# Optimization experiments

Measured on AMD Instinct MI355X. Metric: run time of the kernel, lower is better.

Reference implementation:

```python
import jax, jax.numpy as jnp
import numpy as np

N = 100000   # nodes per node type
E = 400000   # edges per relation
IN = 128     # input feature dim
HID = 128    # hidden_channels
H = 8        # heads
D = HID // H # head dim = 16
NEG_SLOPE = 0.2
BN_EPS = 1e-5


def setup_inputs() -> dict:
    key = jax.random.key(0)
    ks = jax.random.split(key, 24)
    f32 = jnp.float32
    def rn(k, shape, s):
        return jax.random.normal(k, shape, dtype=f32) * s
    inp = {
        'x_a': jax.random.normal(ks[0], (N, IN), dtype=f32),
        'x_b': jax.random.normal(ks[1], (N, IN), dtype=f32),
        'ei_ab': jax.random.randint(ks[2], (2, E), 0, N, dtype=jnp.int32),
        'ei_ba': jax.random.randint(ks[3], (2, E), 0, N, dtype=jnp.int32),
        'ei_aa': jax.random.randint(ks[4], (2, E), 0, N, dtype=jnp.int32),
        'ei_bb': jax.random.randint(ks[5], (2, E), 0, N, dtype=jnp.int32),
        # per-node-type projections (PyG Linear, with bias)
        'W_a': rn(ks[6], (IN, HID), 0.08), 'b_a': jnp.zeros((HID,), f32),
        'W_b': rn(ks[7], (IN, HID), 0.08), 'b_b': jnp.zeros((HID,), f32),
        # per-relation node-level attention vectors [H, D]
        'att_ab_s': rn(ks[8], (H, D), 0.2), 'att_ab_d': rn(ks[9], (H, D), 0.2),
        'att_ba_s': rn(ks[10], (H, D), 0.2), 'att_ba_d': rn(ks[11], (H, D), 0.2),
        'att_aa_s': rn(ks[12], (H, D), 0.2), 'att_aa_d': rn(ks[13], (H, D), 0.2),
        'att_bb_s': rn(ks[14], (H, D), 0.2), 'att_bb_d': rn(ks[15], (H, D), 0.2),
        # semantic-level attention: k_lin (Linear HID->HID) and query q
        'Wk': rn(ks[16], (HID, HID), 0.08), 'bk': jnp.zeros((HID,), f32),
        'q': rn(ks[17], (HID,), 0.2),
        # shared BatchNorm1d affine params
        'gamma': jnp.ones((HID,), f32), 'beta': jnp.zeros((HID,), f32),
    }
    return inp


def _edge_attn(h_src, h_dst, ei, att_s, att_d, n_dst):
    # GAT-style node-level attention for one relation (PyG HANConv message path)
    src, dst = ei[0], ei[1]
    a = (h_src * att_s).sum(-1)[src] + (h_dst * att_d).sum(-1)[dst]  # [E, H]
    a = jax.nn.leaky_relu(a, NEG_SLOPE)
    amax = jax.ops.segment_max(a, dst, num_segments=n_dst)            # [n_dst, H]
    amax = jnp.where(jnp.isfinite(amax), amax, 0.0)
    ex = jnp.exp(a - amax[dst])
    denom = jax.ops.segment_sum(ex, dst, num_segments=n_dst)[dst] + 1e-16
    w = ex / denom                                                    # segment softmax
    out = jax.ops.segment_sum(w[:, :, None] * h_src[src], dst, num_segments=n_dst)
    return jax.nn.relu(out.reshape(n_dst, H * D))                     # [n_dst, HID]


def _semantic(outs, Wk, bk, q):
    # semantic-level attention over relations targeting the same dst type
    st = jnp.stack(outs)                                   # [K, N, HID]
    score = (jnp.tanh(st @ Wk + bk).mean(axis=1) * q).sum(-1)  # [K]
    attn = jax.nn.softmax(score)
    return jnp.einsum('k,knf->nf', attn, st)


def _bn(x, gamma, beta):
    # BatchNorm1d in training mode: batch stats, biased variance
    mu = x.mean(axis=0)
    var = ((x - mu) ** 2).mean(axis=0)
    return (x - mu) * jax.lax.rsqrt(var + BN_EPS) * gamma + beta


def reference(x_a, x_b, ei_ab, ei_ba, ei_aa, ei_bb, W_a, b_a, W_b, b_b,
              att_ab_s, att_ab_d, att_ba_s, att_ba_d, att_aa_s, att_aa_d,
              att_bb_s, att_bb_d, Wk, bk, q, gamma, beta):
    h_a = (x_a @ W_a + b_a).reshape(N, H, D)
    h_b = (x_b @ W_b + b_b).reshape(N, H, D)
    o_ab = _edge_attn(h_a, h_b, ei_ab, att_ab_s, att_ab_d, N)  # dst b
    o_bb = _edge_attn(h_b, h_b, ei_bb, att_bb_s, att_bb_d, N)  # dst b
    o_ba = _edge_attn(h_b, h_a, ei_ba, att_ba_s, att_ba_d, N)  # dst a
    o_aa = _edge_attn(h_a, h_a, ei_aa, att_aa_s, att_aa_d, N)  # dst a
    out_a = _semantic([o_ba, o_aa], Wk, bk, q)
    out_b = _semantic([o_ab, o_bb], Wk, bk, q)
    return _bn(out_a, gamma, beta), _bn(out_b, gamma, beta)
```

## Files before the change

kernel.cpp:

```cpp
#include <hip/hip_runtime.h>

using u16 = unsigned short;
using u32 = unsigned int;
using bf16x8 = __attribute__((ext_vector_type(8))) short;
using f32x4  = __attribute__((ext_vector_type(4))) float;

__device__ __forceinline__ float bf2f(u16 v) { return __uint_as_float(((u32)v) << 16); }
__device__ __forceinline__ float blo(u32 u) { return __uint_as_float(u << 16); }
__device__ __forceinline__ float bhi(u32 u) { return __uint_as_float(u & 0xffff0000u); }
__device__ __forceinline__ u16 f2bf(float f) {
  u32 u = __float_as_uint(f);
  u += 0x7fffu + ((u >> 16) & 1u);
  return (u16)(u >> 16);
}
__device__ __forceinline__ float fast_tanh(float x) {
  float cx = fminf(fmaxf(x, -9.f), 9.f);
  float e = __expf(2.f * cx);
  return (e - 1.f) / (e + 1.f);
}

__global__ __launch_bounds__(256) void wprep_kernel(
    const float* __restrict__ Wa, const float* __restrict__ Wb,
    const float* __restrict__ Wk,
    u16* __restrict__ Ta, u16* __restrict__ Tb, u16* __restrict__ Tk)
{
  const int w = blockIdx.y;
  const float* W = (w == 0) ? Wa : (w == 1) ? Wb : Wk;
  u16* T = (w == 0) ? Ta : (w == 1) ? Tb : Tk;
  int idx = blockIdx.x * 256 + threadIdx.x;
  int k = idx >> 7, n = idx & 127;
  T[n * 128 + k] = f2bf(W[idx]);
}

__global__ __launch_bounds__(256) void proj_kernel(
    const float* __restrict__ x_a, const float* __restrict__ x_b,
    const u16* __restrict__ WTa, const u16* __restrict__ WTb,
    const float* __restrict__ b_a, const float* __restrict__ b_b,
    const float* __restrict__ at0a, const float* __restrict__ at1a,
    const float* __restrict__ at2a, const float* __restrict__ at3a,
    const float* __restrict__ at0b, const float* __restrict__ at1b,
    const float* __restrict__ at2b, const float* __restrict__ at3b,
    u16* __restrict__ ha, u16* __restrict__ hb,
    float* __restrict__ a0a, float* __restrict__ a1a,
    float* __restrict__ a2a, float* __restrict__ a3a,
    float* __restrict__ a0b, float* __restrict__ a1b,
    float* __restrict__ a2b, float* __restrict__ a3b,
    int N)
{
  const int ty = blockIdx.y;
  const float* x   = ty ? x_b : x_a;
  const u16*  WT   = ty ? WTb : WTa;
  const float* bias = ty ? b_b : b_a;
  const float* att0 = ty ? at0b : at0a;
  const float* att1 = ty ? at1b : at1a;
  const float* att2 = ty ? at2b : at2a;
  const float* att3 = ty ? at3b : at3a;
  u16* h_out = ty ? hb : ha;
  float* al0 = ty ? a0b : a0a;
  float* al1 = ty ? a1b : a1a;
  float* al2 = ty ? a2b : a2a;
  float* al3 = ty ? a3b : a3a;

  __shared__ __align__(16) u16 WTl[128 * 136];
  const int tid = threadIdx.x;

  const uint4* Wg = (const uint4*)WT;
#pragma unroll
  for (int i = 0; i < 8; ++i) {
    int id = tid + 256 * i;
    uint4 v = Wg[id];
    int n = id >> 4, k8 = (id & 15) << 3;
    *(uint4*)&WTl[n * 136 + k8] = v;
  }
  __syncthreads();

  const int lane = tid & 63, wl = tid >> 6;
  const int col = lane & 15, g = lane >> 4;
  const int nb = blockIdx.x * 64 + wl * 16;
  const int node = nb + col;
  const bool ok = node < N;

  const int arow = min(node, N - 1);
  const float* xr = x + (size_t)arow * 128;
  bf16x8 xh[4], xlo[4];
#pragma unroll
  for (int t = 0; t < 4; ++t) {
    float4 u = *(const float4*)&xr[t * 32 + g * 8];
    float4 v = *(const float4*)&xr[t * 32 + g * 8 + 4];
    float e[8] = {u.x, u.y, u.z, u.w, v.x, v.y, v.z, v.w};
    bf16x8 h8, l8;
#pragma unroll
    for (int j = 0; j < 8; ++j) {
      u16 hbt = f2bf(e[j]);
      h8[j] = (short)hbt;
      l8[j] = (short)f2bf(e[j] - bf2f(hbt));
    }
    xh[t] = h8; xlo[t] = l8;
  }

  f32x4 acc[8];
#pragma unroll
  for (int c = 0; c < 8; ++c) {
    float4 bv = *(const float4*)&bias[c * 16 + g * 4];
    acc[c] = (f32x4){bv.x, bv.y, bv.z, bv.w};
  }

#pragma unroll
  for (int c = 0; c < 8; ++c) {
    const u16* wrow = &WTl[(c * 16 + col) * 136];
#pragma unroll
    for (int t = 0; t < 4; ++t) {
      bf16x8 wf = *(const bf16x8*)&wrow[t * 32 + g * 8];
      acc[c] = __builtin_amdgcn_mfma_f32_16x16x32_bf16(wf, xh[t],  acc[c], 0, 0, 0);
      acc[c] = __builtin_amdgcn_mfma_f32_16x16x32_bf16(wf, xlo[t], acc[c], 0, 0, 0);
    }
  }

  if (ok) {
#pragma unroll
    for (int c = 0; c < 8; ++c) {
      uint2 hv;
      hv.x = (u32)f2bf(acc[c][0]) | ((u32)f2bf(acc[c][1]) << 16);
      hv.y = (u32)f2bf(acc[c][2]) | ((u32)f2bf(acc[c][3]) << 16);
      *(uint2*)(h_out + (size_t)node * 128 + c * 16 + g * 4) = hv;
    }
  }

#pragma unroll
  for (int c = 0; c < 8; ++c) {
    float4 a0v = *(const float4*)&att0[c * 16 + g * 4];
    float4 a1v = *(const float4*)&att1[c * 16 + g * 4];
    float4 a2v = *(const float4*)&att2[c * 16 + g * 4];
    float4 a3v = *(const float4*)&att3[c * 16 + g * 4];
    float p0 = acc[c][0] * a0v.x + acc[c][1] * a0v.y + acc[c][2] * a0v.z + acc[c][3] * a0v.w;
    float p1 = acc[c][0] * a1v.x + acc[c][1] * a1v.y + acc[c][2] * a1v.z + acc[c][3] * a1v.w;
    float p2 = acc[c][0] * a2v.x + acc[c][1] * a2v.y + acc[c][2] * a2v.z + acc[c][3] * a2v.w;
    float p3 = acc[c][0] * a3v.x + acc[c][1] * a3v.y + acc[c][2] * a3v.z + acc[c][3] * a3v.w;
    p0 += __shfl_xor(p0, 16); p0 += __shfl_xor(p0, 32);
    p1 += __shfl_xor(p1, 16); p1 += __shfl_xor(p1, 32);
    p2 += __shfl_xor(p2, 16); p2 += __shfl_xor(p2, 32);
    p3 += __shfl_xor(p3, 16); p3 += __shfl_xor(p3, 32);
    if (ok && g == 0) {
      al0[node * 8 + c] = p0;
      al1[node * 8 + c] = p1;
      al2[node * 8 + c] = p2;
      al3[node * 8 + c] = p3;
    }
  }
}

__global__ __launch_bounds__(256) void hist_kernel(
    const int* __restrict__ e0, const int* __restrict__ e1,
    const int* __restrict__ e2, const int* __restrict__ e3,
    int E, int N, int* __restrict__ cnt)
{
  const int r = blockIdx.y;
  const int* ei = (r == 0) ? e0 : (r == 1) ? e1 : (r == 2) ? e2 : e3;
  int e = blockIdx.x * 256 + threadIdx.x;
  if (e < E) atomicAdd(&cnt[r * N + ei[E + e]], 1);
}

__global__ __launch_bounds__(256) void scan1_kernel(int* __restrict__ data, int M,
                                                    int* __restrict__ bsum)
{
  __shared__ int ls[256];
  const int tid = threadIdx.x;
  const int base = blockIdx.x * 2048 + tid * 8;
  int v[8]; int s = 0;
#pragma unroll
  for (int j = 0; j < 8; ++j) v[j] = (base + j < M) ? data[base + j] : 0;
#pragma unroll
  for (int j = 0; j < 8; ++j) { int t = v[j]; v[j] = s; s += t; }
  ls[tid] = s;
  __syncthreads();
  for (int off = 1; off < 256; off <<= 1) {
    int t = (tid >= off) ? ls[tid - off] : 0;
    __syncthreads();
    ls[tid] += t;
    __syncthreads();
  }
  int texcl = ls[tid] - s;
#pragma unroll
  for (int j = 0; j < 8; ++j)
    if (base + j < M) data[base + j] = v[j] + texcl;
  if (tid == 255) bsum[blockIdx.x] = ls[255];
}

__global__ __launch_bounds__(256) void scan2_kernel(int* __restrict__ bsum, int G1)
{
  __shared__ int ls[256];
  const int tid = threadIdx.x;
  int v = (tid < G1) ? bsum[tid] : 0;
  ls[tid] = v;
  __syncthreads();
  for (int off = 1; off < 256; off <<= 1) {
    int t = (tid >= off) ? ls[tid - off] : 0;
    __syncthreads();
    ls[tid] += t;
    __syncthreads();
  }
  if (tid < G1) bsum[tid] = ls[tid] - v;
}

__global__ __launch_bounds__(256) void scan3_kernel(int* __restrict__ data,
                                                    const int* __restrict__ bsum, int M,
                                                    int* __restrict__ cursor)
{
  const int add = bsum[blockIdx.x];
  const int base = blockIdx.x * 2048 + threadIdx.x * 8;
#pragma unroll
  for (int j = 0; j < 8; ++j) {
    int i = base + j;
    if (i < M) { int t = data[i] + add; data[i] = t; cursor[i] = t; }
  }
}

__global__ __launch_bounds__(256) void scatter_kernel(
    const int* __restrict__ e0, const int* __restrict__ e1,
    const int* __restrict__ e2, const int* __restrict__ e3,
    int E, int N, int* __restrict__ cursor, int* __restrict__ ssrc)
{
  const int r = blockIdx.y;
  const int* ei = (r == 0) ? e0 : (r == 1) ? e1 : (r == 2) ? e2 : e3;
  int e = blockIdx.x * 256 + threadIdx.x;
  if (e >= E) return;
  int s = ei[e], d = ei[E + e];
  int p = atomicAdd(&cursor[r * N + d], 1);
  ssrc[p] = s;
}

__global__ __launch_bounds__(256) void aggregate_kernel(
    const int* __restrict__ off, const int* __restrict__ ssrc,
    const float* __restrict__ aS0, const float* __restrict__ aS1,
    const float* __restrict__ aS2, const float* __restrict__ aS3,
    const float* __restrict__ aD0, const float* __restrict__ aD1,
    const float* __restrict__ aD2, const float* __restrict__ aD3,
    const u16* __restrict__ h0, const u16* __restrict__ h1,
    const u16* __restrict__ h2, const u16* __restrict__ h3,
    u32* __restrict__ o0, u32* __restrict__ o1,
    u32* __restrict__ o2, u32* __restrict__ o3,
    int N, int E)
{
  const int r = blockIdx.y;
  const float* aS = (r == 0) ? aS0 : (r == 1) ? aS1 : (r == 2) ? aS2 : aS3;
  const float* aD = (r == 0) ? aD0 : (r == 1) ? aD1 : (r == 2) ? aD2 : aD3;
  const u16*   h  = (r == 0) ? h0  : (r == 1) ? h1  : (r == 2) ? h2  : h3;
  u32*         o  = (r == 0) ? o0  : (r == 1) ? o1  : (r == 2) ? o2  : o3;

  const int wave = threadIdx.x >> 6, lane = threadIdx.x & 63;
  const int n = blockIdx.x * 4 + wave;
  if (n >= N) return;
  const int head = lane >> 3;
  const int idx = r * N + n;
  const int p0 = off[idx];
  const int p1 = (idx + 1 < 4 * N) ? off[idx + 1] : 4 * E;
  const float aDv = aD[n * 8 + head];
  const u32* h32 = (const u32*)h;

  float acc0 = 0.f, acc1 = 0.f, den = 0.f;
  int p = p0;
  for (; p + 4 <= p1; p += 4) {
    const int s0 = ssrc[p], s1 = ssrc[p + 1], s2 = ssrc[p + 2], s3 = ssrc[p + 3];
    const float g0 = aS[s0 * 8 + head];
    const float g1 = aS[s1 * 8 + head];
    const float g2 = aS[s2 * 8 + head];
    const float g3 = aS[s3 * 8 + head];
    const u32 v0 = h32[s0 * 64 + lane];
    const u32 v1 = h32[s1 * 64 + lane];
    const u32 v2 = h32[s2 * 64 + lane];
    const u32 v3 = h32[s3 * 64 + lane];
    float l0 = g0 + aDv, l1 = g1 + aDv, l2 = g2 + aDv, l3 = g3 + aDv;
    l0 = fmaxf(l0, 0.2f * l0); l1 = fmaxf(l1, 0.2f * l1);
    l2 = fmaxf(l2, 0.2f * l2); l3 = fmaxf(l3, 0.2f * l3);
    const float w0 = __expf(l0), w1 = __expf(l1);
    const float w2 = __expf(l2), w3 = __expf(l3);
    den += (w0 + w1) + (w2 + w3);
    acc0 += w0 * blo(v0) + w1 * blo(v1) + w2 * blo(v2) + w3 * blo(v3);
    acc1 += w0 * bhi(v0) + w1 * bhi(v1) + w2 * bhi(v2) + w3 * bhi(v3);
  }
  const int rem = p1 - p;
  if (rem > 0) {
    const int s0 = ssrc[p];
    const int s1 = ssrc[(rem > 1) ? p + 1 : p];
    const int s2 = ssrc[(rem > 2) ? p + 2 : p];
    const float g0 = aS[s0 * 8 + head];
    const float g1 = aS[s1 * 8 + head];
    const float g2 = aS[s2 * 8 + head];
    const u32 v0 = h32[s0 * 64 + lane];
    const u32 v1 = h32[s1 * 64 + lane];
    const u32 v2 = h32[s2 * 64 + lane];
    float l0 = g0 + aDv, l1 = g1 + aDv, l2 = g2 + aDv;
    l0 = fmaxf(l0, 0.2f * l0); l1 = fmaxf(l1, 0.2f * l1); l2 = fmaxf(l2, 0.2f * l2);
    const float w0 = __expf(l0);
    const float w1 = (rem > 1) ? __expf(l1) : 0.f;
    const float w2 = (rem > 2) ? __expf(l2) : 0.f;
    den += w0 + w1 + w2;
    acc0 += w0 * blo(v0) + w1 * blo(v1) + w2 * blo(v2);
    acc1 += w0 * bhi(v0) + w1 * bhi(v1) + w2 * bhi(v2);
  }
  const float inv = 1.f / (den + 1e-16f);
  const float r0 = fmaxf(acc0 * inv, 0.f);
  const float r1 = fmaxf(acc1 * inv, 0.f);
  o[n * 64 + lane] = (u32)f2bf(r0) | ((u32)f2bf(r1) << 16);
}

__global__ __launch_bounds__(256) void sem_score_kernel(
    const u16* __restrict__ oba, const u16* __restrict__ oaa,
    const u16* __restrict__ oab, const u16* __restrict__ obb,
    const u16* __restrict__ WkT, const float* __restrict__ bk,
    const float* __restrict__ q, float* __restrict__ scores, int N)
{
  const int rel = blockIdx.y;
  const u16* o = (rel == 0) ? oba : (rel == 1) ? oaa : (rel == 2) ? oab : obb;

  __shared__ __align__(16) u16 WTl[128 * 136];
  __shared__ float red[4];
  const int tid = threadIdx.x;

  const uint4* Wg = (const uint4*)WkT;
#pragma unroll
  for (int i = 0; i < 8; ++i) {
    int id = tid + 256 * i;
    uint4 v = Wg[id];
    int n = id >> 4, k8 = (id & 15) << 3;
    *(uint4*)&WTl[n * 136 + k8] = v;
  }
  __syncthreads();

  const int lane = tid & 63, wl = tid >> 6;
  const int col = lane & 15, g = lane >> 4;
  const int nb = blockIdx.x * 64 + wl * 16;

  float bv[8], qv[8];
#pragma unroll
  for (int c = 0; c < 8; ++c) {
    bv[c] = bk[c * 16 + col];
    qv[c] = q[c * 16 + col];
  }

  const int arow = min(nb + col, N - 1);
  const u16* orow = o + (size_t)arow * 128;
  bf16x8 af[4];
#pragma unroll
  for (int t = 0; t < 4; ++t) af[t] = *(const bf16x8*)&orow[t * 32 + g * 8];

  f32x4 acc[8];
#pragma unroll
  for (int c = 0; c < 8; ++c) acc[c] = (f32x4){bv[c], bv[c], bv[c], bv[c]};

#pragma unroll
  for (int c = 0; c < 8; ++c) {
    const u16* wrow = &WTl[(c * 16 + col) * 136];
#pragma unroll
    for (int t = 0; t < 4; ++t) {
      bf16x8 bf = *(const bf16x8*)&wrow[t * 32 + g * 8];
      acc[c] = __builtin_amdgcn_mfma_f32_16x16x32_bf16(af[t], bf, acc[c], 0, 0, 0);
    }
  }

  float p = 0.f;
  const int rowbase = nb + g * 4;
#pragma unroll
  for (int c = 0; c < 8; ++c) {
#pragma unroll
    for (int i = 0; i < 4; ++i) {
      int node = rowbase + i;
      if (node < N) p += fast_tanh(acc[c][i]) * qv[c];
    }
  }
#pragma unroll
  for (int off = 32; off > 0; off >>= 1) p += __shfl_down(p, off);
  if (lane == 0) red[wl] = p;
  __syncthreads();
  if (tid == 0) atomicAdd(&scores[rel], red[0] + red[1] + red[2] + red[3]);
}

__global__ void attn_kernel(const float* __restrict__ scores, float* __restrict__ attn,
                            float invN)
{
  if (threadIdx.x == 0) {
#pragma unroll
    for (int t = 0; t < 2; ++t) {
      float s0 = scores[2 * t] * invN, s1 = scores[2 * t + 1] * invN;
      float m = fmaxf(s0, s1);
      float e0 = expf(s0 - m), e1 = expf(s1 - m);
      float inv = 1.f / (e0 + e1);
      attn[2 * t] = e0 * inv; attn[2 * t + 1] = e1 * inv;
    }
  }
}

__global__ __launch_bounds__(256) void bn_stats_kernel(
    const u32* __restrict__ oba, const u32* __restrict__ oaa,
    const u32* __restrict__ oab, const u32* __restrict__ obb,
    const float* __restrict__ attn, float* __restrict__ sums_a,
    float* __restrict__ sums_b, int N, int R)
{
  const int t = blockIdx.y;
  const u32* o0 = t ? oab : oba;
  const u32* o1 = t ? obb : oaa;
  const float* at = attn + 2 * t;
  float* sums = t ? sums_b : sums_a;

  const float a0 = at[0], a1 = at[1];
  const int tid = threadIdx.x;
  const int tc = tid & 31;
  const int tr = tid >> 5;
  float s[4] = {0.f, 0.f, 0.f, 0.f}, sq[4] = {0.f, 0.f, 0.f, 0.f};
  const int rend = min((blockIdx.x + 1) * R, N);
  for (int row = blockIdx.x * R + tr; row < rend; row += 8) {
    uint2 v0 = *(const uint2*)&o0[row * 64 + tc * 2];
    uint2 v1 = *(const uint2*)&o1[row * 64 + tc * 2];
    float c0 = a0 * blo(v0.x) + a1 * blo(v1.x);
    float c1 = a0 * bhi(v0.x) + a1 * bhi(v1.x);
    float c2 = a0 * blo(v0.y) + a1 * blo(v1.y);
    float c3 = a0 * bhi(v0.y) + a1 * bhi(v1.y);
    s[0] += c0; sq[0] += c0 * c0;
    s[1] += c1; sq[1] += c1 * c1;
    s[2] += c2; sq[2] += c2 * c2;
    s[3] += c3; sq[3] += c3 * c3;
  }
  __shared__ float sacc[128], sqacc[128];
  if (tid < 128) { sacc[tid] = 0.f; sqacc[tid] = 0.f; }
  __syncthreads();
#pragma unroll
  for (int j = 0; j < 4; ++j) {
    atomicAdd(&sacc[tc * 4 + j], s[j]);
    atomicAdd(&sqacc[tc * 4 + j], sq[j]);
  }
  __syncthreads();
  if (tid < 128) {
    atomicAdd(&sums[tid], sacc[tid]);
    atomicAdd(&sums[128 + tid], sqacc[tid]);
  }
}

__global__ __launch_bounds__(256) void bn_final_kernel(
    const u32* __restrict__ oba, const u32* __restrict__ oaa,
    const u32* __restrict__ oab, const u32* __restrict__ obb,
    const float* __restrict__ attn, const float* __restrict__ sums_a,
    const float* __restrict__ sums_b,
    const float* __restrict__ gamma, const float* __restrict__ beta,
    float* __restrict__ out, int N)
{
  const int t = blockIdx.y;
  const u32* o0 = t ? oab : oba;
  const u32* o1 = t ? obb : oaa;
  const float* at = attn + 2 * t;
  const float* sums = t ? sums_b : sums_a;
  float* op = out + (size_t)t * N * 128;

  __shared__ float scale[128], shift[128];
  if (threadIdx.x < 128) {
    int f = threadIdx.x;
    float invN = 1.f / (float)N;
    float mu = sums[f] * invN;
    float var = fmaxf(sums[128 + f] * invN - mu * mu, 0.f);
    float rs = rsqrtf(var + 1e-5f);
    float g = gamma[f] * rs;
    scale[f] = g;
    shift[f] = beta[f] - mu * g;
  }
  const float a0 = at[0], a1 = at[1];
  __syncthreads();
  size_t total = (size_t)N * 128;
  for (size_t base = ((size_t)blockIdx.x * 256 + threadIdx.x) * 8; base < total;
       base += (size_t)gridDim.x * 2048) {
    int f0 = (int)(base & 127);
    uint4 p = *(const uint4*)&o0[base >> 1];
    uint4 q = *(const uint4*)&o1[base >> 1];
    float4 r0, r1;
    r0.x = (a0 * blo(p.x) + a1 * blo(q.x)) * scale[f0 + 0] + shift[f0 + 0];
    r0.y = (a0 * bhi(p.x) + a1 * bhi(q.x)) * scale[f0 + 1] + shift[f0 + 1];
    r0.z = (a0 * blo(p.y) + a1 * blo(q.y)) * scale[f0 + 2] + shift[f0 + 2];
    r0.w = (a0 * bhi(p.y) + a1 * bhi(q.y)) * scale[f0 + 3] + shift[f0 + 3];
    r1.x = (a0 * blo(p.z) + a1 * blo(q.z)) * scale[f0 + 4] + shift[f0 + 4];
    r1.y = (a0 * bhi(p.z) + a1 * bhi(q.z)) * scale[f0 + 5] + shift[f0 + 5];
    r1.z = (a0 * blo(p.w) + a1 * blo(q.w)) * scale[f0 + 6] + shift[f0 + 6];
    r1.w = (a0 * bhi(p.w) + a1 * bhi(q.w)) * scale[f0 + 7] + shift[f0 + 7];
    *(float4*)&op[base] = r0;
    *(float4*)&op[base + 4] = r1;
  }
}

extern "C" void kernel_launch(void* const* d_in, const int* in_sizes, int n_in,
                              void* d_out, int out_size, void* d_ws, size_t ws_size,
                              hipStream_t stream)
{
  const float* x_a      = (const float*)d_in[0];
  const float* x_b      = (const float*)d_in[1];
  const int* ei_ab      = (const int*)d_in[2];
  const int* ei_ba      = (const int*)d_in[3];
  const int* ei_aa      = (const int*)d_in[4];
  const int* ei_bb      = (const int*)d_in[5];
  const float* W_a      = (const float*)d_in[6];
  const float* b_a      = (const float*)d_in[7];
  const float* W_b      = (const float*)d_in[8];
  const float* b_b      = (const float*)d_in[9];
  const float* att_ab_s = (const float*)d_in[10];
  const float* att_ab_d = (const float*)d_in[11];
  const float* att_ba_s = (const float*)d_in[12];
  const float* att_ba_d = (const float*)d_in[13];
  const float* att_aa_s = (const float*)d_in[14];
  const float* att_aa_d = (const float*)d_in[15];
  const float* att_bb_s = (const float*)d_in[16];
  const float* att_bb_d = (const float*)d_in[17];
  const float* Wk       = (const float*)d_in[18];
  const float* bk       = (const float*)d_in[19];
  const float* q        = (const float*)d_in[20];
  const float* gamma    = (const float*)d_in[21];
  const float* beta     = (const float*)d_in[22];

  const int N = in_sizes[0] / 128;
  const int E = in_sizes[2] / 2;

  char* wp = (char*)d_ws;
  auto alloc = [&](size_t bytes) -> void* {
    void* p = (void*)wp;
    wp += (bytes + 255) & ~(size_t)255;
    return p;
  };
  u16* h_a = (u16*)alloc((size_t)N * 128 * 2);
  u16* h_b = (u16*)alloc((size_t)N * 128 * 2);
  float* A[8];
  for (int i = 0; i < 8; ++i) A[i] = (float*)alloc((size_t)N * 8 * 4);
  int* off    = (int*)alloc((size_t)4 * N * 4);
  int* cursor = (int*)alloc((size_t)4 * N * 4);
  int* bsum   = (int*)alloc(1024);
  int* ssrc   = (int*)alloc((size_t)4 * E * 4);
  u32* o_ab = (u32*)alloc((size_t)N * 64 * 4);
  u32* o_ba = (u32*)alloc((size_t)N * 64 * 4);
  u32* o_aa = (u32*)alloc((size_t)N * 64 * 4);
  u32* o_bb = (u32*)alloc((size_t)N * 64 * 4);
  float* scores = (float*)alloc(16);
  float* attn   = (float*)alloc(16);
  float* sums_a = (float*)alloc(1024);
  float* sums_b = (float*)alloc(1024);
  u16* WT_a = (u16*)alloc(128 * 128 * 2);
  u16* WT_b = (u16*)alloc(128 * 128 * 2);
  u16* WT_k = (u16*)alloc(128 * 128 * 2);
  if ((size_t)(wp - (char*)d_ws) > ws_size) return;

  hipMemsetAsync(off, 0, (size_t)4 * N * 4, stream);
  hipMemsetAsync(scores, 0, 2560, stream);

  dim3 gw(64, 3);
  wprep_kernel<<<gw, 256, 0, stream>>>(W_a, W_b, Wk, WT_a, WT_b, WT_k);

  const int gproj = (N + 63) / 64;
  dim3 gp(gproj, 2);
  proj_kernel<<<gp, 256, 0, stream>>>(
      x_a, x_b, WT_a, WT_b, b_a, b_b,
      att_ab_s, att_aa_s, att_aa_d, att_ba_d,
      att_ab_d, att_bb_s, att_bb_d, att_ba_s,
      h_a, h_b,
      A[0], A[1], A[2], A[3], A[4], A[5], A[6], A[7], N);

  const int gE = (E + 255) / 256;
  dim3 gh(gE, 4);
  hist_kernel<<<gh, 256, 0, stream>>>(ei_ab, ei_ba, ei_aa, ei_bb, E, N, off);
  const int M = 4 * N;
  const int G1 = (M + 2047) / 2048;
  scan1_kernel<<<G1, 256, 0, stream>>>(off, M, bsum);
  scan2_kernel<<<1, 256, 0, stream>>>(bsum, G1);
  scan3_kernel<<<G1, 256, 0, stream>>>(off, bsum, M, cursor);
  dim3 gsc(gE, 4);
  scatter_kernel<<<gsc, 256, 0, stream>>>(ei_ab, ei_ba, ei_aa, ei_bb, E, N, cursor, ssrc);

  dim3 gag((N + 3) / 4, 4);
  aggregate_kernel<<<gag, 256, 0, stream>>>(
      off, ssrc,
      A[0], A[7], A[1], A[5],
      A[4], A[3], A[2], A[6],
      h_a, h_b, h_a, h_b,
      o_ab, o_ba, o_aa, o_bb, N, E);

  dim3 gsem(gproj, 4);
  sem_score_kernel<<<gsem, 256, 0, stream>>>(
      (const u16*)o_ba, (const u16*)o_aa, (const u16*)o_ab, (const u16*)o_bb,
      WT_k, bk, q, scores, N);
  attn_kernel<<<1, 64, 0, stream>>>(scores, attn, 1.0f / (float)N);

  const int R = (N + 255) / 256;
  dim3 gbs(256, 2);
  bn_stats_kernel<<<gbs, 256, 0, stream>>>(o_ba, o_aa, o_ab, o_bb, attn,
                                           sums_a, sums_b, N, R);
  float* out = (float*)d_out;
  dim3 gbf(1024, 2);
  bn_final_kernel<<<gbf, 256, 0, stream>>>(o_ba, o_aa, o_ab, o_bb, attn,
                                           sums_a, sums_b, gamma, beta, out, N);
}
```

Measured before the change: 696.6 us.

## Fuse projection, histogram and weight prep; compute BN stats independently of attention

The weight-prep, projection and edge-histogram kernels become one launch whose block roles are interleaved, with W_a/W_b converted to bf16 directly in shared memory. The semantic-score and BN-stats passes are merged into a single launch. This works because BN statistics are now gathered as per-relation sums, squares and cross-products, so the mean and variance can be rebuilt once the attention weights are known. The separate attn kernel is folded into bn_final. This removes several launches and serialization points and lets independent work overlap, at the cost of redundant per-block W conversion and more atomics.

```diff
diff --git a/kernel.cpp b/kernel.cpp
--- a/kernel.cpp
+++ b/kernel.cpp
@@ -19,22 +19,9 @@
   return (e - 1.f) / (e + 1.f);
 }
 
-__global__ __launch_bounds__(256) void wprep_kernel(
-    const float* __restrict__ Wa, const float* __restrict__ Wb,
-    const float* __restrict__ Wk,
-    u16* __restrict__ Ta, u16* __restrict__ Tb, u16* __restrict__ Tk)
-{
-  const int w = blockIdx.y;
-  const float* W = (w == 0) ? Wa : (w == 1) ? Wb : Wk;
-  u16* T = (w == 0) ? Ta : (w == 1) ? Tb : Tk;
-  int idx = blockIdx.x * 256 + threadIdx.x;
-  int k = idx >> 7, n = idx & 127;
-  T[n * 128 + k] = f2bf(W[idx]);
-}
-
-__global__ __launch_bounds__(256) void proj_kernel(
+__global__ __launch_bounds__(256) void fused1_kernel(
     const float* __restrict__ x_a, const float* __restrict__ x_b,
-    const u16* __restrict__ WTa, const u16* __restrict__ WTb,
+    const float* __restrict__ W_a, const float* __restrict__ W_b,
     const float* __restrict__ b_a, const float* __restrict__ b_b,
     const float* __restrict__ at0a, const float* __restrict__ at1a,
     const float* __restrict__ at2a, const float* __restrict__ at3a,
@@ -45,11 +32,46 @@
     float* __restrict__ a2a, float* __restrict__ a3a,
     float* __restrict__ a0b, float* __restrict__ a1b,
     float* __restrict__ a2b, float* __restrict__ a3b,
-    int N)
-{
-  const int ty = blockIdx.y;
-  const float* x   = ty ? x_b : x_a;
-  const u16*  WT   = ty ? WTb : WTa;
+    const int* __restrict__ e0, const int* __restrict__ e1,
+    const int* __restrict__ e2, const int* __restrict__ e3,
+    const float* __restrict__ Wk, u16* __restrict__ WkT,
+    int* __restrict__ cnt,
+    int N, int E, int gproj, int gE, int interleave)
+{
+  __shared__ __align__(16) u16 WTl[128 * 136];
+  const int tid = threadIdx.x;
+  const int bid = blockIdx.x;
+  const int nP = 2 * gproj, nH = 4 * gE;
+
+  int role, idx;
+  if (bid >= nP + nH) { role = 2; idx = bid - nP - nH; }
+  else if (interleave) {
+    int slot = bid % 3, grp = bid / 3;
+    if (slot == 0) { role = 0; idx = grp; }
+    else           { role = 1; idx = grp * 2 + slot - 1; }
+  } else {
+    if (bid < nP) { role = 0; idx = bid; }
+    else          { role = 1; idx = bid - nP; }
+  }
+
+  if (role == 1) {
+    const int r = idx & 3, ex = idx >> 2;
+    const int* ei = (r == 0) ? e0 : (r == 1) ? e1 : (r == 2) ? e2 : e3;
+    int e = ex * 256 + tid;
+    if (e < E) atomicAdd(&cnt[r * N + ei[E + e]], 1);
+    return;
+  }
+  if (role == 2) {
+    int i2 = idx * 256 + tid;
+    int k = i2 >> 7, n = i2 & 127;
+    WkT[n * 128 + k] = f2bf(Wk[i2]);
+    return;
+  }
+
+  const int ty = idx >= gproj;
+  const int bx = idx - (ty ? gproj : 0);
+  const float* x    = ty ? x_b : x_a;
+  const float* W    = ty ? W_b : W_a;
   const float* bias = ty ? b_b : b_a;
   const float* att0 = ty ? at0b : at0a;
   const float* att1 = ty ? at1b : at1a;
@@ -61,22 +83,22 @@
   float* al2 = ty ? a2b : a2a;
   float* al3 = ty ? a3b : a3a;
 
-  __shared__ __align__(16) u16 WTl[128 * 136];
-  const int tid = threadIdx.x;
-
-  const uint4* Wg = (const uint4*)WT;
-#pragma unroll
-  for (int i = 0; i < 8; ++i) {
+  const float4* Wg = (const float4*)W;
+#pragma unroll
+  for (int i = 0; i < 16; ++i) {
     int id = tid + 256 * i;
-    uint4 v = Wg[id];
-    int n = id >> 4, k8 = (id & 15) << 3;
-    *(uint4*)&WTl[n * 136 + k8] = v;
+    int k = id >> 5, n4 = (id & 31) << 2;
+    float4 v = Wg[id];
+    WTl[(n4 + 0) * 136 + k] = f2bf(v.x);
+    WTl[(n4 + 1) * 136 + k] = f2bf(v.y);
+    WTl[(n4 + 2) * 136 + k] = f2bf(v.z);
+    WTl[(n4 + 3) * 136 + k] = f2bf(v.w);
   }
   __syncthreads();
 
   const int lane = tid & 63, wl = tid >> 6;
   const int col = lane & 15, g = lane >> 4;
-  const int nb = blockIdx.x * 64 + wl * 16;
+  const int nb = bx * 64 + wl * 16;
   const int node = nb + col;
   const bool ok = node < N;
 
@@ -147,17 +169,6 @@
       al3[node * 8 + c] = p3;
     }
   }
-}
-
-__global__ __launch_bounds__(256) void hist_kernel(
-    const int* __restrict__ e0, const int* __restrict__ e1,
-    const int* __restrict__ e2, const int* __restrict__ e3,
-    int E, int N, int* __restrict__ cnt)
-{
-  const int r = blockIdx.y;
-  const int* ei = (r == 0) ? e0 : (r == 1) ? e1 : (r == 2) ? e2 : e3;
-  int e = blockIdx.x * 256 + threadIdx.x;
-  if (e < E) atomicAdd(&cnt[r * N + ei[E + e]], 1);
 }
 
 __global__ __launch_bounds__(256) void scan1_kernel(int* __restrict__ data, int M,
@@ -304,18 +315,61 @@
   o[n * 64 + lane] = (u32)f2bf(r0) | ((u32)f2bf(r1) << 16);
 }
 
-__global__ __launch_bounds__(256) void sem_score_kernel(
-    const u16* __restrict__ oba, const u16* __restrict__ oaa,
-    const u16* __restrict__ oab, const u16* __restrict__ obb,
+__global__ __launch_bounds__(256) void fused2_kernel(
+    const u32* __restrict__ oba, const u32* __restrict__ oaa,
+    const u32* __restrict__ oab, const u32* __restrict__ obb,
     const u16* __restrict__ WkT, const float* __restrict__ bk,
-    const float* __restrict__ q, float* __restrict__ scores, int N)
-{
-  const int rel = blockIdx.y;
-  const u16* o = (rel == 0) ? oba : (rel == 1) ? oaa : (rel == 2) ? oab : obb;
-
+    const float* __restrict__ q, float* __restrict__ scores,
+    float* __restrict__ sums_a, float* __restrict__ sums_b,
+    int N, int R, int gproj)
+{
   __shared__ __align__(16) u16 WTl[128 * 136];
   __shared__ float red[4];
   const int tid = threadIdx.x;
+  const int bid = blockIdx.x;
+
+  if (bid < 512) {
+    const int t = bid >> 8, bx = bid & 255;
+    const u32* p0 = t ? oab : oba;
+    const u32* p1 = t ? obb : oaa;
+    float* sums = t ? sums_b : sums_a;
+    const int tc = tid & 31, tr = tid >> 5;
+    float s0[4] = {0,0,0,0}, s1[4] = {0,0,0,0};
+    float q00[4] = {0,0,0,0}, q11[4] = {0,0,0,0}, q01[4] = {0,0,0,0};
+    const int rend = min((bx + 1) * R, N);
+    for (int row = bx * R + tr; row < rend; row += 8) {
+      uint2 v0 = *(const uint2*)&p0[row * 64 + tc * 2];
+      uint2 v1 = *(const uint2*)&p1[row * 64 + tc * 2];
+      float r0[4] = {blo(v0.x), bhi(v0.x), blo(v0.y), bhi(v0.y)};
+      float r1[4] = {blo(v1.x), bhi(v1.x), blo(v1.y), bhi(v1.y)};
+#pragma unroll
+      for (int j = 0; j < 4; ++j) {
+        s0[j] += r0[j]; s1[j] += r1[j];
+        q00[j] += r0[j] * r0[j]; q11[j] += r1[j] * r1[j];
+        q01[j] += r0[j] * r1[j];
+      }
+    }
+    float* sm = (float*)WTl;
+    for (int i = tid; i < 640; i += 256) sm[i] = 0.f;
+    __syncthreads();
+#pragma unroll
+    for (int j = 0; j < 4; ++j) {
+      int f = tc * 4 + j;
+      atomicAdd(&sm[f], s0[j]);
+      atomicAdd(&sm[128 + f], s1[j]);
+      atomicAdd(&sm[256 + f], q00[j]);
+      atomicAdd(&sm[384 + f], q11[j]);
+      atomicAdd(&sm[512 + f], q01[j]);
+    }
+    __syncthreads();
+    for (int i = tid; i < 640; i += 256) atomicAdd(&sums[i], sm[i]);
+    return;
+  }
+
+  const int sid = bid - 512;
+  const int rel = sid & 3, bx = sid >> 2;
+  const u32* op = (rel == 0) ? oba : (rel == 1) ? oaa : (rel == 2) ? oab : obb;
+  const u16* o = (const u16*)op;
 
   const uint4* Wg = (const uint4*)WkT;
 #pragma unroll
@@ -329,7 +383,7 @@
 
   const int lane = tid & 63, wl = tid >> 6;
   const int col = lane & 15, g = lane >> 4;
-  const int nb = blockIdx.x * 64 + wl * 16;
+  const int nb = bx * 64 + wl * 16;
 
   float bv[8], qv[8];
 #pragma unroll
@@ -375,93 +429,40 @@
   if (tid == 0) atomicAdd(&scores[rel], red[0] + red[1] + red[2] + red[3]);
 }
 
-__global__ void attn_kernel(const float* __restrict__ scores, float* __restrict__ attn,
-                            float invN)
-{
-  if (threadIdx.x == 0) {
-#pragma unroll
-    for (int t = 0; t < 2; ++t) {
-      float s0 = scores[2 * t] * invN, s1 = scores[2 * t + 1] * invN;
-      float m = fmaxf(s0, s1);
-      float e0 = expf(s0 - m), e1 = expf(s1 - m);
-      float inv = 1.f / (e0 + e1);
-      attn[2 * t] = e0 * inv; attn[2 * t + 1] = e1 * inv;
-    }
-  }
-}
-
-__global__ __launch_bounds__(256) void bn_stats_kernel(
+__global__ __launch_bounds__(256) void bn_final_kernel(
     const u32* __restrict__ oba, const u32* __restrict__ oaa,
     const u32* __restrict__ oab, const u32* __restrict__ obb,
-    const float* __restrict__ attn, float* __restrict__ sums_a,
-    float* __restrict__ sums_b, int N, int R)
+    const float* __restrict__ scores, const float* __restrict__ sums_a,
+    const float* __restrict__ sums_b,
+    const float* __restrict__ gamma, const float* __restrict__ beta,
+    float* __restrict__ out, int N)
 {
   const int t = blockIdx.y;
   const u32* o0 = t ? oab : oba;
   const u32* o1 = t ? obb : oaa;
-  const float* at = attn + 2 * t;
-  float* sums = t ? sums_b : sums_a;
-
-  const float a0 = at[0], a1 = at[1];
-  const int tid = threadIdx.x;
-  const int tc = tid & 31;
-  const int tr = tid >> 5;
-  float s[4] = {0.f, 0.f, 0.f, 0.f}, sq[4] = {0.f, 0.f, 0.f, 0.f};
-  const int rend = min((blockIdx.x + 1) * R, N);
-  for (int row = blockIdx.x * R + tr; row < rend; row += 8) {
-    uint2 v0 = *(const uint2*)&o0[row * 64 + tc * 2];
-    uint2 v1 = *(const uint2*)&o1[row * 64 + tc * 2];
-    float c0 = a0 * blo(v0.x) + a1 * blo(v1.x);
-    float c1 = a0 * bhi(v0.x) + a1 * bhi(v1.x);
-    float c2 = a0 * blo(v0.y) + a1 * blo(v1.y);
-    float c3 = a0 * bhi(v0.y) + a1 * bhi(v1.y);
-    s[0] += c0; sq[0] += c0 * c0;
-    s[1] += c1; sq[1] += c1 * c1;
-    s[2] += c2; sq[2] += c2 * c2;
-    s[3] += c3; sq[3] += c3 * c3;
-  }
-  __shared__ float sacc[128], sqacc[128];
-  if (tid < 128) { sacc[tid] = 0.f; sqacc[tid] = 0.f; }
-  __syncthreads();
-#pragma unroll
-  for (int j = 0; j < 4; ++j) {
-    atomicAdd(&sacc[tc * 4 + j], s[j]);
-    atomicAdd(&sqacc[tc * 4 + j], sq[j]);
-  }
-  __syncthreads();
-  if (tid < 128) {
-    atomicAdd(&sums[tid], sacc[tid]);
-    atomicAdd(&sums[128 + tid], sqacc[tid]);
-  }
-}
-
-__global__ __launch_bounds__(256) void bn_final_kernel(
-    const u32* __restrict__ oba, const u32* __restrict__ oaa,
-    const u32* __restrict__ oab, const u32* __restrict__ obb,
-    const float* __restrict__ attn, const float* __restrict__ sums_a,
-    const float* __restrict__ sums_b,
-    const float* __restrict__ gamma, const float* __restrict__ beta,
-    float* __restrict__ out, int N)
-{
-  const int t = blockIdx.y;
-  const u32* o0 = t ? oab : oba;
-  const u32* o1 = t ? obb : oaa;
-  const float* at = attn + 2 * t;
   const float* sums = t ? sums_b : sums_a;
   float* op = out + (size_t)t * N * 128;
+
+  const float invN = 1.f / (float)N;
+  const float sc0 = scores[2 * t] * invN, sc1 = scores[2 * t + 1] * invN;
+  const float m = fmaxf(sc0, sc1);
+  const float e0 = expf(sc0 - m), e1 = expf(sc1 - m);
+  const float einv = 1.f / (e0 + e1);
+  const float a0 = e0 * einv, a1 = e1 * einv;
 
   __shared__ float scale[128], shift[128];
   if (threadIdx.x < 128) {
     int f = threadIdx.x;
-    float invN = 1.f / (float)N;
-    float mu = sums[f] * invN;
-    float var = fmaxf(sums[128 + f] * invN - mu * mu, 0.f);
+    float S0 = sums[f], S1 = sums[128 + f];
+    float Q00 = sums[256 + f], Q11 = sums[384 + f], Q01 = sums[512 + f];
+    float mu = (a0 * S0 + a1 * S1) * invN;
+    float msq = (a0 * a0 * Q00 + 2.f * a0 * a1 * Q01 + a1 * a1 * Q11) * invN;
+    float var = fmaxf(msq - mu * mu, 0.f);
     float rs = rsqrtf(var + 1e-5f);
-    float g = gamma[f] * rs;
-    scale[f] = g;
-    shift[f] = beta[f] - mu * g;
-  }
-  const float a0 = at[0], a1 = at[1];
+    float gm = gamma[f] * rs;
+    scale[f] = gm;
+    shift[f] = beta[f] - mu * gm;
+  }
   __syncthreads();
   size_t total = (size_t)N * 128;
   for (size_t base = ((size_t)blockIdx.x * 256 + threadIdx.x) * 8; base < total;
@@ -533,32 +534,27 @@
   u32* o_aa = (u32*)alloc((size_t)N * 64 * 4);
   u32* o_bb = (u32*)alloc((size_t)N * 64 * 4);
   float* scores = (float*)alloc(16);
-  float* attn   = (float*)alloc(16);
-  float* sums_a = (float*)alloc(1024);
-  float* sums_b = (float*)alloc(1024);
-  u16* WT_a = (u16*)alloc(128 * 128 * 2);
-  u16* WT_b = (u16*)alloc(128 * 128 * 2);
+  float* sums_a = (float*)alloc(2560);
+  float* sums_b = (float*)alloc(2560);
   u16* WT_k = (u16*)alloc(128 * 128 * 2);
   if ((size_t)(wp - (char*)d_ws) > ws_size) return;
 
   hipMemsetAsync(off, 0, (size_t)4 * N * 4, stream);
-  hipMemsetAsync(scores, 0, 2560, stream);
-
-  dim3 gw(64, 3);
-  wprep_kernel<<<gw, 256, 0, stream>>>(W_a, W_b, Wk, WT_a, WT_b, WT_k);
+  hipMemsetAsync(scores, 0, 5376, stream);
 
   const int gproj = (N + 63) / 64;
-  dim3 gp(gproj, 2);
-  proj_kernel<<<gp, 256, 0, stream>>>(
-      x_a, x_b, WT_a, WT_b, b_a, b_b,
+  const int gE = (E + 255) / 256;
+  const int interleave = (gE == gproj) ? 1 : 0;
+  const int g1total = 2 * gproj + 4 * gE + 64;
+  fused1_kernel<<<g1total, 256, 0, stream>>>(
+      x_a, x_b, W_a, W_b, b_a, b_b,
       att_ab_s, att_aa_s, att_aa_d, att_ba_d,
       att_ab_d, att_bb_s, att_bb_d, att_ba_s,
       h_a, h_b,
-      A[0], A[1], A[2], A[3], A[4], A[5], A[6], A[7], N);
-
-  const int gE = (E + 255) / 256;
-  dim3 gh(gE, 4);
-  hist_kernel<<<gh, 256, 0, stream>>>(ei_ab, ei_ba, ei_aa, ei_bb, E, N, off);
+      A[0], A[1], A[2], A[3], A[4], A[5], A[6], A[7],
+      ei_ab, ei_ba, ei_aa, ei_bb,
+      Wk, WT_k, off, N, E, gproj, gE, interleave);
+
   const int M = 4 * N;
   const int G1 = (M + 2047) / 2048;
   scan1_kernel<<<G1, 256, 0, stream>>>(off, M, bsum);
@@ -575,18 +571,13 @@
       h_a, h_b, h_a, h_b,
       o_ab, o_ba, o_aa, o_bb, N, E);
 
-  dim3 gsem(gproj, 4);
-  sem_score_kernel<<<gsem, 256, 0, stream>>>(
-      (const u16*)o_ba, (const u16*)o_aa, (const u16*)o_ab, (const u16*)o_bb,
-      WT_k, bk, q, scores, N);
-  attn_kernel<<<1, 64, 0, stream>>>(scores, attn, 1.0f / (float)N);
-
   const int R = (N + 255) / 256;
-  dim3 gbs(256, 2);
-  bn_stats_kernel<<<gbs, 256, 0, stream>>>(o_ba, o_aa, o_ab, o_bb, attn,
-                                           sums_a, sums_b, N, R);
+  const int g2total = 512 + 4 * gproj;
+  fused2_kernel<<<g2total, 256, 0, stream>>>(
+      o_ba, o_aa, o_ab, o_bb, WT_k, bk, q, scores, sums_a, sums_b, N, R, gproj);
+
   float* out = (float*)d_out;
   dim3 gbf(1024, 2);
-  bn_final_kernel<<<gbf, 256, 0, stream>>>(o_ba, o_aa, o_ab, o_bb, attn,
+  bn_final_kernel<<<gbf, 256, 0, stream>>>(o_ba, o_aa, o_ab, o_bb, scores,
                                            sums_a, sums_b, gamma, beta, out, N);
 }
```

After: 654.3 us. 1.06x faster.
